# Performance work log

Hardware: AMD Instinct MI355X
Metric: run time of the kernel (lower is better)

Reference implementation:

```python
import jax, jax.numpy as jnp
import numpy as np

B, S, D = 32, 1, 2048
H, KVH, HD = 16, 4, 128
MAXS = 4096
EPS = 1e-5
NREP = H // KVH  # GQA repeat factor = 4
FF = 4 * D
POS = 4095  # decode position (start_pos)


def setup_inputs() -> dict:
    key = jax.random.key(0)
    ks = jax.random.split(key, 12)
    sc = lambda d: 1.0 / np.sqrt(d)
    # RoPE angles for the current token position, [S, HD//2]
    inv_freq = 1.0 / (10000.0 ** (np.arange(0, HD, 2, dtype=np.float32) / HD))
    ang = (POS + np.arange(S, dtype=np.float32))[:, None] * inv_freq[None, :]
    return {
        "x": jax.random.normal(ks[0], (B, S, D), jnp.float32),
        "cos": jnp.asarray(np.cos(ang), jnp.float32),
        "sin": jnp.asarray(np.sin(ang), jnp.float32),
        "k_cache": jax.random.normal(ks[1], (B, MAXS, KVH, HD), jnp.float32),
        "v_cache": jax.random.normal(ks[2], (B, MAXS, KVH, HD), jnp.float32),
        "w_rms_attn": jnp.ones((D,), jnp.float32),
        "wq": jax.random.normal(ks[3], (D, D), jnp.float32) * sc(D),
        "wk": jax.random.normal(ks[4], (D, KVH * HD), jnp.float32) * sc(D),
        "wv": jax.random.normal(ks[5], (D, KVH * HD), jnp.float32) * sc(D),
        "wo": jax.random.normal(ks[6], (D, D), jnp.float32) * sc(D),
        "w_rms_ffn": jnp.ones((D,), jnp.float32),
        "w1": jax.random.normal(ks[7], (D, FF), jnp.float32) * sc(D),
        "w2": jax.random.normal(ks[8], (D, FF), jnp.float32) * sc(D),
        "w3": jax.random.normal(ks[9], (FF, D), jnp.float32) * sc(FF),
        "start_pos": POS,
    }


def _rmsnorm(x, g):
    return x * g * jax.lax.rsqrt(jnp.mean(x * x, axis=-1, keepdims=True) + EPS)


def _rope(x, cos, sin):
    # x: [B, S, h, HD]; complex rotation on (even, odd) pairs
    xr = x.reshape(*x.shape[:-1], HD // 2, 2)
    x0, x1 = xr[..., 0], xr[..., 1]
    c = cos[None, :, None, :]
    s = sin[None, :, None, :]
    r0 = x0 * c - x1 * s
    r1 = x0 * s + x1 * c
    return jnp.stack([r0, r1], axis=-1).reshape(x.shape)


def reference(x, cos, sin, k_cache, v_cache, w_rms_attn, wq, wk, wv, wo,
              w_rms_ffn, w1, w2, w3, start_pos):
    xa = _rmsnorm(x, w_rms_attn)
    xq = (xa @ wq).reshape(B, S, H, HD)
    xk = (xa @ wk).reshape(B, S, KVH, HD)
    xv = (xa @ wv).reshape(B, S, KVH, HD)
    # Source applies RoPE to K and V (not Q) -- reproduced faithfully.
    xk = _rope(xk, cos, sin)
    xv = _rope(xv, cos, sin)
    kc = jax.lax.dynamic_update_slice(k_cache, xk, (0, start_pos, 0, 0))
    vc = jax.lax.dynamic_update_slice(v_cache, xv, (0, start_pos, 0, 0))
    klen = start_pos + S
    keys = jnp.repeat(kc[:, :klen], NREP, axis=2)   # [B, klen, H, HD]
    vals = jnp.repeat(vc[:, :klen], NREP, axis=2)
    att = jnp.einsum('bqhd,bkhd->bhqk', xq, keys) * (HD ** -0.5)
    att = jax.nn.softmax(att, axis=-1)
    y = jnp.einsum('bhqk,bkhd->bqhd', att, vals).reshape(B, S, D)
    h = x + y @ wo
    xf = _rmsnorm(h, w_rms_ffn)
    return h + (jax.nn.silu(xf @ w1) * (xf @ w2)) @ w3
```

## Files before the change

### kernel.cpp

```cpp
#include <hip/hip_runtime.h>
#include <math.h>

#define BB 32
#define DD 2048
#define NKVH 4
#define HDIM 128
#define MAXS 4096
#define FFD 8192
#define POS 4095
#define EPSV 1e-5f
#define SCALE 0.08838834764831845f
#define ASPLIT 32
#define SPOS 128

#define OFF_QN   0u
#define OFF_KN   65536u
#define OFF_VN   81920u
#define OFF_G1   98304u
#define OFF_G2   360448u
#define ZERO_N   622592u
#define OFF_XAT  622592u
#define OFF_PML  720896u
#define OFF_PACC 753664u
#define OFF_YT   2850816u
#define OFF_H    2916352u
#define OFF_XFT  2981888u

#define VM_WAIT8  asm volatile("s_waitcnt vmcnt(8)" ::: "memory")
#define VM_WAIT0  asm volatile("s_waitcnt vmcnt(0)" ::: "memory")
#define LG_WAIT0  asm volatile("s_waitcnt lgkmcnt(0)" ::: "memory")
#define SCHED0    __builtin_amdgcn_sched_barrier(0)
#define SBAR      __builtin_amdgcn_s_barrier()

#define REP32(M) M(0) M(1) M(2) M(3) M(4) M(5) M(6) M(7) M(8) M(9) M(10) M(11) M(12) M(13) M(14) M(15) M(16) M(17) M(18) M(19) M(20) M(21) M(22) M(23) M(24) M(25) M(26) M(27) M(28) M(29) M(30) M(31)
#define REP32A(M,X) M(0,X) M(1,X) M(2,X) M(3,X) M(4,X) M(5,X) M(6,X) M(7,X) M(8,X) M(9,X) M(10,X) M(11,X) M(12,X) M(13,X) M(14,X) M(15,X) M(16,X) M(17,X) M(18,X) M(19,X) M(20,X) M(21,X) M(22,X) M(23,X) M(24,X) M(25,X) M(26,X) M(27,X) M(28,X) M(29,X) M(30,X) M(31,X)

#define DECLA(i) float a##i = 0.f;
#define FMA1(i,k) a##i = fmaf(ap[(k)*32 + (i)], w##k, a##i);
#define STORET(i) tl[i] = a##i;
#define ATOMN(i) atomicAdd(C + (size_t)(i)*N + n, a##i);

template<int N, int CH, bool TOUT>
__device__ __forceinline__ void gemv_body(const float* __restrict__ At,
                                          const float* __restrict__ W,
                                          float* __restrict__ C, int colblk,
                                          float* tile) {
    int tid = (int)threadIdx.x;
    int n = colblk * 256 + tid;
    int d0 = blockIdx.y * CH;
    const float* Wp = W + (size_t)d0 * N + n;
    const float* ap = At + (size_t)d0 * 32;
    REP32(DECLA)
#pragma unroll 4
    for (int dd = 0; dd < CH; dd += 4) {
        float w0 = Wp[0];
        float w1 = Wp[(size_t)N];
        float w2 = Wp[(size_t)N * 2];
        float w3 = Wp[(size_t)N * 3];
        REP32A(FMA1, 0)
        REP32A(FMA1, 1)
        REP32A(FMA1, 2)
        REP32A(FMA1, 3)
        Wp += (size_t)N * 4;
        ap += 128;
    }
    if constexpr (TOUT) {
        float* tl = tile + tid * 33;
        REP32(STORET)
        __syncthreads();
        float* cb = C + (size_t)colblk * 256 * 32;
#pragma unroll
        for (int i = 0; i < 32; ++i) {
            int f = i * 256 + tid;
            atomicAdd(cb + f, tile[(f >> 5) * 33 + (f & 31)]);
        }
    } else {
        REP32(ATOMN)
    }
}

template<int N, int CH, bool TOUT>
__global__ __launch_bounds__(256) void gemv32_kernel(const float* __restrict__ At,
                                                     const float* __restrict__ W,
                                                     float* __restrict__ C) {
    if constexpr (TOUT) {
        __shared__ float tile[256 * 33];
        gemv_body<N, CH, true>(At, W, C, blockIdx.x, tile);
    } else {
        gemv_body<N, CH, false>(At, W, C, blockIdx.x, nullptr);
    }
}

template<int N, int CH, int HALF>
__global__ __launch_bounds__(256) void gemv32_dual_kernel(const float* __restrict__ At,
        const float* __restrict__ W0, const float* __restrict__ W1,
        float* __restrict__ C0, float* __restrict__ C1) {
    __shared__ float tile[256 * 33];
    int bx = blockIdx.x;
    if (bx < HALF) gemv_body<8192, CH, true>(At, W0, C0, bx, tile);
    else           gemv_body<8192, CH, true>(At, W1, C1, bx - HALF, tile);
}

__global__ __launch_bounds__(256) void gemv_qkv_kernel(const float* __restrict__ At,
        const float* __restrict__ wq, const float* __restrict__ wk,
        const float* __restrict__ wv, float* __restrict__ qn,
        float* __restrict__ kn, float* __restrict__ vn) {
    int bx = blockIdx.x;
    if (bx < 8)       gemv_body<2048, 32, false>(At, wq, qn, bx, nullptr);
    else if (bx < 10) gemv_body<512, 32, false>(At, wk, kn, bx - 8, nullptr);
    else              gemv_body<512, 32, false>(At, wv, vn, bx - 10, nullptr);
}

__global__ void zero_rms_kernel(float* __restrict__ p, const float* __restrict__ in,
                                const float* __restrict__ g, float* __restrict__ outT,
                                float* __restrict__ cpy) {
    int bx = blockIdx.x, tid = threadIdx.x;
    if (bx < 608) {
        ((float4*)p)[bx * 256 + tid] = (float4){0.f, 0.f, 0.f, 0.f};
        return;
    }
    int b = bx - 608;
    const float* row = in + b * DD;
    float v[8];
    float ss = 0.f;
#pragma unroll
    for (int i = 0; i < 8; ++i) { v[i] = row[tid + i * 256]; ss += v[i] * v[i]; }
#pragma unroll
    for (int off = 32; off; off >>= 1) ss += __shfl_xor(ss, off);
    __shared__ float red[4];
    if ((tid & 63) == 0) red[tid >> 6] = ss;
    __syncthreads();
    ss = red[0] + red[1] + red[2] + red[3];
    float scale = rsqrtf(ss * (1.f / DD) + EPSV);
#pragma unroll
    for (int i = 0; i < 8; ++i) {
        int idx = tid + i * 256;
        outT[(size_t)idx * 32 + b] = v[i] * g[idx] * scale;
        cpy[b * DD + idx] = v[i];
    }
}

__global__ void rmsnorm_kernel(const float* __restrict__ in, const float* __restrict__ g,
                               float* __restrict__ outT, float* __restrict__ cpy) {
    int b = blockIdx.x;
    int tid = threadIdx.x;
    const float* row = in + b * DD;
    float v[8];
    float ss = 0.f;
#pragma unroll
    for (int i = 0; i < 8; ++i) { v[i] = row[tid + i * 256]; ss += v[i] * v[i]; }
#pragma unroll
    for (int off = 32; off; off >>= 1) ss += __shfl_xor(ss, off);
    __shared__ float red[4];
    if ((tid & 63) == 0) red[tid >> 6] = ss;
    __syncthreads();
    ss = red[0] + red[1] + red[2] + red[3];
    float scale = rsqrtf(ss * (1.f / DD) + EPSV);
#pragma unroll
    for (int i = 0; i < 8; ++i) {
        int idx = tid + i * 256;
        outT[(size_t)idx * 32 + b] = v[i] * g[idx] * scale;
        if (cpy) cpy[b * DD + idx] = v[i];
    }
}

__global__ __launch_bounds__(256, 2) void attn_stage_kernel(
    const float* __restrict__ qn, const float* __restrict__ kc, const float* __restrict__ vc,
    const float* __restrict__ kn, const float* __restrict__ vn,
    const float* __restrict__ cosb, const float* __restrict__ sinb,
    float* __restrict__ pml, float* __restrict__ pacc) {
    int split = blockIdx.x & 31, b = blockIdx.x >> 5;
    int tid = threadIdx.x, lane = tid & 63, wv = tid >> 6;
    __shared__ float kbuf[2][8192];
    __shared__ float p_s[128][16];
    int qpos = tid >> 4, qhead = tid & 15;
    int qr = qpos * 4 + (qhead >> 2);
    int vh = tid >> 4, c16 = tid & 15, vkvh = vh >> 2;
    int t0 = split * SPOS;

    float4 qrot[32];
#pragma unroll
    for (int j = 0; j < 32; ++j) {
        int g = (j + qr) & 31;
        qrot[j] = *(const float4*)(qn + (size_t)b * DD + qhead * HDIM + g * 4);
    }
    float4 av0 = {0, 0, 0, 0}, av1 = {0, 0, 0, 0};

    auto stage = [&](int t) {
        int s = t & 7;
        const float* base = (t < 8) ? kc + ((size_t)b * MAXS + t0 + s * 16) * 512
                                    : vc + ((size_t)b * MAXS + t0 + s * 16) * 512;
        const float* g = base + wv * 2048 + lane * 4;
        float* l = &kbuf[t & 1][wv * 2048];
        int imax = (split == 31 && s == 7 && wv == 3) ? 6 : 8;
#pragma unroll
        for (int i = 0; i < 8; ++i)
            if (i < imax)
                __builtin_amdgcn_global_load_lds(
                    (const __attribute__((address_space(1))) void*)(g + i * 256),
                    (__attribute__((address_space(3))) void*)(l + i * 256), 16, 0, 0);
    };

    stage(0);
    for (int t = 0; t < 16; ++t) {
        if (t < 15) {
            stage(t + 1);
            if (split == 31 && wv == 3 && (t == 6 || t == 14)) {
                const float* src = (t == 6) ? kn : vn;
                float* dst = &kbuf[(t + 1) & 1][7680 + lane * 8];
                int col0 = lane * 8;
#pragma unroll
                for (int m = 0; m < 4; ++m) {
                    int col = col0 + 2 * m;
                    int ci = (col & 127) >> 1;
                    float cc = cosb[ci], ssn = sinb[ci];
                    float x0 = src[b * 512 + col], x1 = src[b * 512 + col + 1];
                    dst[2 * m]     = x0 * cc - x1 * ssn;
                    dst[2 * m + 1] = x0 * ssn + x1 * cc;
                }
            }
            VM_WAIT8;
        } else { VM_WAIT0; }
        SCHED0; SBAR;
        if (t == 8) {
#pragma unroll
            for (int hh = 0; hh < 4; ++hh) {
                int h = wv * 4 + hh;
                float e0 = p_s[lane][h], e1 = p_s[lane + 64][h];
                float m = fmaxf(e0, e1);
#pragma unroll
                for (int off = 32; off; off >>= 1) m = fmaxf(m, __shfl_xor(m, off));
                e0 = __expf(e0 - m); e1 = __expf(e1 - m);
                p_s[lane][h] = e0; p_s[lane + 64][h] = e1;
                float l2 = e0 + e1;
#pragma unroll
                for (int off = 32; off; off >>= 1) l2 += __shfl_xor(l2, off);
                if (lane == 0) {
                    int idx = ((b * ASPLIT + split) * 16 + h) * 2;
                    pml[idx] = m; pml[idx + 1] = l2;
                }
            }
        }
        const float* kb = kbuf[t & 1];
        if (t < 8) {
            float4 acc = {0, 0, 0, 0};
            const float* rowp = kb + qr * 128;
#pragma unroll
            for (int j = 0; j < 32; ++j) {
                int g = (j + qr) & 31;
                float4 k4 = *(const float4*)(rowp + g * 4);
                acc.x = fmaf(k4.x, qrot[j].x, acc.x);
                acc.y = fmaf(k4.y, qrot[j].y, acc.y);
                acc.z = fmaf(k4.z, qrot[j].z, acc.z);
                acc.w = fmaf(k4.w, qrot[j].w, acc.w);
            }
            p_s[t * 16 + qpos][qhead] = (acc.x + acc.y + acc.z + acc.w) * SCALE;
        } else {
            int s = t - 8;
            const float* vrow = kb + vkvh * 128 + c16 * 4;
#pragma unroll
            for (int p = 0; p < 16; ++p) {
                float pw = p_s[s * 16 + p][vh];
                float4 v0 = *(const float4*)(vrow + p * 512);
                float4 v1 = *(const float4*)(vrow + p * 512 + 64);
                av0.x = fmaf(pw, v0.x, av0.x); av0.y = fmaf(pw, v0.y, av0.y);
                av0.z = fmaf(pw, v0.z, av0.z); av0.w = fmaf(pw, v0.w, av0.w);
                av1.x = fmaf(pw, v1.x, av1.x); av1.y = fmaf(pw, v1.y, av1.y);
                av1.z = fmaf(pw, v1.z, av1.z); av1.w = fmaf(pw, v1.w, av1.w);
            }
        }
        LG_WAIT0; SCHED0; SBAR;
    }
    size_t pbase = ((size_t)(b * ASPLIT + split) * 16 + vh) * HDIM;
    *(float4*)(pacc + pbase + c16 * 4) = av0;
    *(float4*)(pacc + pbase + 64 + c16 * 4) = av1;
}

__global__ void attn_combine_kernel(const float* __restrict__ pml,
                                    const float* __restrict__ pacc, float* __restrict__ yT) {
    int bid = blockIdx.x;
    int b = bid >> 4, h = bid & 15;
    int d = threadIdx.x;
    float M = -INFINITY;
#pragma unroll 8
    for (int s = 0; s < ASPLIT; ++s)
        M = fmaxf(M, pml[((b * ASPLIT + s) * 16 + h) * 2]);
    float denom = 0.f, acc = 0.f;
#pragma unroll 4
    for (int s = 0; s < ASPLIT; ++s) {
        int idx = (b * ASPLIT + s) * 16 + h;
        float e = __expf(pml[idx * 2] - M);
        denom += pml[idx * 2 + 1] * e;
        acc += e * pacc[(size_t)idx * HDIM + d];
    }
    yT[(size_t)(h * HDIM + d) * 32 + b] = acc / denom;
}

__global__ void silu_mul_kernel(float* __restrict__ g1, const float* __restrict__ g2) {
    int i = blockIdx.x * 256 + threadIdx.x;
    float4 a = ((const float4*)g1)[i];
    float4 b4 = ((const float4*)g2)[i];
    a.x = a.x * b4.x / (1.f + __expf(-a.x));
    a.y = a.y * b4.y / (1.f + __expf(-a.y));
    a.z = a.z * b4.z / (1.f + __expf(-a.z));
    a.w = a.w * b4.w / (1.f + __expf(-a.w));
    ((float4*)g1)[i] = a;
}

extern "C" void kernel_launch(void* const* d_in, const int* in_sizes, int n_in,
                              void* d_out, int out_size, void* d_ws, size_t ws_size,
                              hipStream_t stream) {
    (void)in_sizes; (void)n_in; (void)out_size; (void)ws_size;
    const float* x    = (const float*)d_in[0];
    const float* cosb = (const float*)d_in[1];
    const float* sinb = (const float*)d_in[2];
    const float* kc   = (const float*)d_in[3];
    const float* vc   = (const float*)d_in[4];
    const float* wra  = (const float*)d_in[5];
    const float* wq   = (const float*)d_in[6];
    const float* wk   = (const float*)d_in[7];
    const float* wv   = (const float*)d_in[8];
    const float* wo   = (const float*)d_in[9];
    const float* wrf  = (const float*)d_in[10];
    const float* w1   = (const float*)d_in[11];
    const float* w2   = (const float*)d_in[12];
    const float* w3   = (const float*)d_in[13];
    float* out = (float*)d_out;
    float* ws  = (float*)d_ws;

    float* qn   = ws + OFF_QN;
    float* kn   = ws + OFF_KN;
    float* vn   = ws + OFF_VN;
    float* g1T  = ws + OFF_G1;
    float* g2T  = ws + OFF_G2;
    float* xaT  = ws + OFF_XAT;
    float* pml  = ws + OFF_PML;
    float* pacc = ws + OFF_PACC;
    float* yT   = ws + OFF_YT;
    float* h    = ws + OFF_H;
    float* xfT  = ws + OFF_XFT;

    zero_rms_kernel<<<640, 256, 0, stream>>>(ws, x, wra, xaT, h);
    gemv_qkv_kernel<<<dim3(12, 64), 256, 0, stream>>>(xaT, wq, wk, wv, qn, kn, vn);
    attn_stage_kernel<<<1024, 256, 0, stream>>>(qn, kc, vc, kn, vn, cosb, sinb, pml, pacc);
    attn_combine_kernel<<<512, 128, 0, stream>>>(pml, pacc, yT);
    gemv32_kernel<2048, 32, false><<<dim3(8, 64), 256, 0, stream>>>(yT, wo, h);
    rmsnorm_kernel<<<32, 256, 0, stream>>>(h, wrf, xfT, out);
    gemv32_dual_kernel<8192, 128, 32><<<dim3(64, 16), 256, 0, stream>>>(xfT, w1, w2, g1T, g2T);
    silu_mul_kernel<<<256, 256, 0, stream>>>(g1T, g2T);
    gemv32_kernel<2048, 128, false><<<dim3(8, 64), 256, 0, stream>>>(g1T, w3, out);
}
```

Baseline: 292.2 us.

## Stream FFN weights into LDS via direct global-to-LDS loads with double buffering

Replaces the register-based weight loads in the FFN up/gate and down projection GEMVs with global_load_lds direct-to-LDS transfers into a double-buffered 8-row tile, then reads weights from LDS for the FMA loop. The goal is to keep more weight bytes in flight and overlap memory fetch with compute in these bandwidth-bound kernels. It adds block barriers per tile and extra LDS use, which can lower occupancy. The old dual GEMV kernel and the TOUT branch of the plain kernel are removed.

```diff
diff --git a/kernel.cpp b/kernel.cpp
--- a/kernel.cpp
+++ b/kernel.cpp
@@ -27,6 +27,7 @@
 #define OFF_XFT  2981888u
 
 #define VM_WAIT8  asm volatile("s_waitcnt vmcnt(8)" ::: "memory")
+#define VM_WAIT2  asm volatile("s_waitcnt vmcnt(2)" ::: "memory")
 #define VM_WAIT0  asm volatile("s_waitcnt vmcnt(0)" ::: "memory")
 #define LG_WAIT0  asm volatile("s_waitcnt lgkmcnt(0)" ::: "memory")
 #define SCHED0    __builtin_amdgcn_sched_barrier(0)
@@ -37,6 +38,7 @@
 
 #define DECLA(i) float a##i = 0.f;
 #define FMA1(i,k) a##i = fmaf(ap[(k)*32 + (i)], w##k, a##i);
+#define FMAR(i) a##i = fmaf(apr[(i)], wl, a##i);
 #define STORET(i) tl[i] = a##i;
 #define ATOMN(i) atomicAdd(C + (size_t)(i)*N + n, a##i);
 
@@ -83,22 +85,7 @@
 __global__ __launch_bounds__(256) void gemv32_kernel(const float* __restrict__ At,
                                                      const float* __restrict__ W,
                                                      float* __restrict__ C) {
-    if constexpr (TOUT) {
-        __shared__ float tile[256 * 33];
-        gemv_body<N, CH, true>(At, W, C, blockIdx.x, tile);
-    } else {
-        gemv_body<N, CH, false>(At, W, C, blockIdx.x, nullptr);
-    }
-}
-
-template<int N, int CH, int HALF>
-__global__ __launch_bounds__(256) void gemv32_dual_kernel(const float* __restrict__ At,
-        const float* __restrict__ W0, const float* __restrict__ W1,
-        float* __restrict__ C0, float* __restrict__ C1) {
-    __shared__ float tile[256 * 33];
-    int bx = blockIdx.x;
-    if (bx < HALF) gemv_body<8192, CH, true>(At, W0, C0, bx, tile);
-    else           gemv_body<8192, CH, true>(At, W1, C1, bx - HALF, tile);
+    gemv_body<N, CH, false>(At, W, C, blockIdx.x, nullptr);
 }
 
 __global__ __launch_bounds__(256) void gemv_qkv_kernel(const float* __restrict__ At,
@@ -109,6 +96,74 @@
     if (bx < 8)       gemv_body<2048, 32, false>(At, wq, qn, bx, nullptr);
     else if (bx < 10) gemv_body<512, 32, false>(At, wk, kn, bx - 8, nullptr);
     else              gemv_body<512, 32, false>(At, wv, vn, bx - 10, nullptr);
+}
+
+template<int N, int CH, bool TOUT>
+__device__ __forceinline__ void gemv_dma_body(const float* __restrict__ At,
+                                              const float* __restrict__ W,
+                                              float* __restrict__ C, int cb,
+                                              float (*wbuf)[8][256], float* tile) {
+    int tid = (int)threadIdx.x, lane = tid & 63, wv = tid >> 6;
+    int d0 = blockIdx.y * CH;
+    constexpr int NT = CH / 8;
+    const float* ap = At + (size_t)d0 * 32;
+    REP32(DECLA)
+    auto stage = [&](int t) {
+        const float* g = W + (size_t)(d0 + t * 8 + wv * 2) * N + cb * 256 + lane * 4;
+        float* l = &wbuf[t & 1][wv * 2][lane * 4];
+        __builtin_amdgcn_global_load_lds(
+            (const __attribute__((address_space(1))) void*)g,
+            (__attribute__((address_space(3))) void*)l, 16, 0, 0);
+        __builtin_amdgcn_global_load_lds(
+            (const __attribute__((address_space(1))) void*)(g + N),
+            (__attribute__((address_space(3))) void*)(l + 256), 16, 0, 0);
+    };
+    stage(0);
+    for (int t = 0; t < NT; ++t) {
+        if (t + 1 < NT) { stage(t + 1); VM_WAIT2; } else { VM_WAIT0; }
+        SCHED0; SBAR;
+        const float* wb = &wbuf[t & 1][0][0];
+#pragma unroll
+        for (int r = 0; r < 8; ++r) {
+            float wl = wb[r * 256 + tid];
+            const float* apr = ap + (t * 8 + r) * 32;
+            REP32(FMAR)
+        }
+        SBAR;
+    }
+    int n = cb * 256 + tid;
+    if constexpr (TOUT) {
+        float* tl = tile + tid * 33;
+        REP32(STORET)
+        __syncthreads();
+        float* cbp = C + (size_t)cb * 256 * 32;
+#pragma unroll
+        for (int i = 0; i < 32; ++i) {
+            int f = i * 256 + tid;
+            atomicAdd(cbp + f, tile[(f >> 5) * 33 + (f & 31)]);
+        }
+    } else {
+        REP32(ATOMN)
+    }
+}
+
+template<int N, int CH>
+__global__ __launch_bounds__(256) void gemv_dma_kernel(const float* __restrict__ At,
+                                                       const float* __restrict__ W,
+                                                       float* __restrict__ C) {
+    __shared__ float wbuf[2][8][256];
+    gemv_dma_body<N, CH, false>(At, W, C, blockIdx.x, wbuf, nullptr);
+}
+
+template<int CH, int HALF>
+__global__ __launch_bounds__(256) void gemv_dma_dual_kernel(const float* __restrict__ At,
+        const float* __restrict__ W0, const float* __restrict__ W1,
+        float* __restrict__ C0, float* __restrict__ C1) {
+    __shared__ float wbuf[2][8][256];
+    __shared__ float tile[256 * 33];
+    int bx = blockIdx.x;
+    if (bx < HALF) gemv_dma_body<8192, CH, true>(At, W0, C0, bx, wbuf, tile);
+    else           gemv_dma_body<8192, CH, true>(At, W1, C1, bx - HALF, wbuf, tile);
 }
 
 __global__ void zero_rms_kernel(float* __restrict__ p, const float* __restrict__ in,
@@ -346,7 +401,7 @@
     attn_combine_kernel<<<512, 128, 0, stream>>>(pml, pacc, yT);
     gemv32_kernel<2048, 32, false><<<dim3(8, 64), 256, 0, stream>>>(yT, wo, h);
     rmsnorm_kernel<<<32, 256, 0, stream>>>(h, wrf, xfT, out);
-    gemv32_dual_kernel<8192, 128, 32><<<dim3(64, 16), 256, 0, stream>>>(xfT, w1, w2, g1T, g2T);
+    gemv_dma_dual_kernel<128, 32><<<dim3(64, 16), 256, 0, stream>>>(xfT, w1, w2, g1T, g2T);
     silu_mul_kernel<<<256, 256, 0, stream>>>(g1T, g2T);
-    gemv32_kernel<2048, 128, false><<<dim3(8, 64), 256, 0, stream>>>(g1T, w3, out);
-}
+    gemv_dma_kernel<2048, 128><<<dim3(8, 64), 256, 0, stream>>>(g1T, w3, out);
+}
```

New measurement: 307.4 us. 1.05x slower.
